# Optimization experiments

Measured on AMD Instinct MI355X. Metric: run time of the kernel, lower is better.

Reference implementation:

```python
import jax, jax.numpy as jnp
import numpy as np

BS, NS, NSTEP = 128, 1024, 8
IN_DIM, HID, MLP = 768, 512, 512
NEG = -100000.0


def setup_inputs() -> dict:
    key = jax.random.key(0)
    ks = jax.random.split(key, 12)
    s_h = 1.0 / np.sqrt(HID)
    s_cat = 1.0 / np.sqrt(HID + IN_DIM)
    s_m = 1.0 / np.sqrt(MLP)
    # gumbel noise implements Categorical sampling as argmax(logits + gumbel)
    u = jax.random.uniform(ks[9], (NSTEP, BS, NS), jnp.float32, 1e-7, 1.0 - 1e-7)
    return {
        "target_emb": jax.random.normal(ks[0], (BS, IN_DIM), jnp.float32),
        "ctx_emb": jax.random.normal(ks[1], (BS, NS, IN_DIM), jnp.float32),
        "target_len": jax.random.randint(ks[2], (BS,), 1, 32),
        "ctx_len": jax.random.randint(ks[3], (BS,), NSTEP, NS + 1),
        "n_step": NSTEP,
        "W_ih": jax.random.normal(ks[4], (4 * HID, IN_DIM), jnp.float32) * s_h,
        "W_hh": jax.random.normal(ks[5], (4 * HID, HID), jnp.float32) * s_h,
        "b_ih": jnp.zeros((4 * HID,), jnp.float32),
        "b_hh": jnp.zeros((4 * HID,), jnp.float32),
        "W1c": jax.random.normal(ks[6], (MLP, IN_DIM), jnp.float32) * s_cat,
        "W1h": jax.random.normal(ks[7], (MLP, HID), jnp.float32) * s_cat,
        "b1": jnp.zeros((MLP,), jnp.float32),
        "w2": jax.random.normal(ks[8], (MLP,), jnp.float32) * s_m,
        "b2": jnp.zeros((), jnp.float32),
        "gumbel": -jnp.log(-jnp.log(u)),
    }


def reference(target_emb, ctx_emb, target_len, ctx_len, n_step,
              W_ih, W_hh, b_ih, b_hh, W1c, W1h, b1, w2, b2, gumbel):
    bs, ns, in_dim = ctx_emb.shape
    hid = W_hh.shape[1]
    # mlp1 split: ctx part is constant across steps (concat([ctx, h]) @ W1^T = ctx@W1c^T + h@W1h^T)
    ctx_part = jnp.einsum('bnd,md->bnm', ctx_emb, W1c) + b1  # [bs, ns, mlp]
    mask0 = jnp.where(jnp.arange(ns)[None, :] >= ctx_len[:, None], NEG, 0.0).astype(jnp.float32)
    h0 = jnp.zeros((bs, hid), jnp.float32)
    c0 = jnp.zeros((bs, hid), jnp.float32)
    lp0 = jnp.zeros((bs,), jnp.float32)
    batch_idx = jnp.arange(bs)

    def step(carry, g):
        h, c, mask, x, lp = carry
        # LSTMCell (torch gate order: i, f, g, o); dropout is identity (eval semantics)
        gates = x @ W_ih.T + b_ih + h @ W_hh.T + b_hh
        i_g, f_g, g_g, o_g = jnp.split(gates, 4, axis=-1)
        c_new = jax.nn.sigmoid(f_g) * c + jax.nn.sigmoid(i_g) * jnp.tanh(g_g)
        h_new = jax.nn.sigmoid(o_g) * jnp.tanh(c_new)
        # attention-style MLP score
        pre = ctx_part + (h_new @ W1h.T)[:, None, :]          # [bs, ns, mlp]
        sc = jnp.tanh(pre) @ w2 + b2 + mask                   # [bs, ns]
        # Categorical(probs=softmax(sc)).sample() via Gumbel-argmax
        out = jnp.argmax(sc + g, axis=-1)                     # [bs]
        lp = lp + jnp.take_along_axis(jax.nn.log_softmax(sc, axis=-1), out[:, None], 1)[:, 0]
        mask = mask.at[batch_idx, out].set(NEG)
        x_new = jnp.take_along_axis(ctx_emb, out[:, None, None], axis=1)[:, 0, :]
        return (h_new, c_new, mask, x_new, lp), out

    (h, c, mask, x, log_probs), outputs = jax.lax.scan(
        step, (h0, c0, mask0, target_emb, lp0), gumbel)
    return outputs, log_probs
```

## Files before the change

### kernel.cpp

```cpp
#include <hip/hip_runtime.h>
#include <hip/hip_bf16.h>

#define BSZ 128
#define NSQ 1024
#define NSTEPC 8
#define IND 768
#define HIDD 512
#define G4D 2048
#define MLPD 512
#define KXD 1280
#define NEGV -100000.0f
#define KSG 16
#define KSH 8
#define MSPLIT 4

typedef __attribute__((ext_vector_type(4))) float f32x4;
typedef __attribute__((ext_vector_type(8))) short short8v;

__device__ __forceinline__ void gl16(const unsigned short* g, unsigned short* l) {
  __builtin_amdgcn_global_load_lds(
      (const __attribute__((address_space(1))) unsigned int*)(g),
      (__attribute__((address_space(3))) unsigned int*)(l), 16, 0, 0);
}

__device__ __forceinline__ void split2(float4 f0, float4 f1, short8v& hi, short8v& lo) {
  float fv[8] = {f0.x, f0.y, f0.z, f0.w, f1.x, f1.y, f1.z, f1.w};
#pragma unroll
  for (int j = 0; j < 8; ++j) {
    const unsigned ub = __builtin_bit_cast(unsigned, fv[j]);
    const unsigned hb = ub & 0xFFFF0000u;
    const float lf = fv[j] - __builtin_bit_cast(float, hb);
    hi[j] = (short)(hb >> 16);
    lo[j] = (short)(__builtin_bit_cast(unsigned, lf) >> 16);
  }
}

__device__ __forceinline__ float tanh_fast(float x) {
  x = fminf(fmaxf(x, -15.0f), 15.0f);
  float e = __builtin_amdgcn_exp2f(x * 2.8853900817779268f);
  float r = __builtin_amdgcn_rcpf(e + 1.0f);
  return fmaf(-2.0f, r, 1.0f);
}

__global__ __launch_bounds__(256) void k_prep_w1c(
    const float* __restrict__ W1c,
    unsigned short* __restrict__ wch, unsigned short* __restrict__ wcl) {
  const int c = blockIdx.x * 256 + threadIdx.x;
  if (c >= 49152) return;
  const int row = c / 96, wc = c - row * 96;
  const int tile = wc >> 2, c4 = wc & 3;
  const int slot = c4 ^ ((row >> 1) & 3);
  const size_t unit = ((size_t)((row >> 7) * 24 + tile) * 128 + (row & 127)) * 4 + slot;
  const float* src = W1c + (size_t)row * IND + wc * 8;
  const float4 f0 = *(const float4*)src, f1 = *(const float4*)(src + 4);
  short8v hi, lo;
  split2(f0, f1, hi, lo);
  *(short8v*)(wch + unit * 8) = hi;
  *(short8v*)(wcl + unit * 8) = lo;
}

__global__ __launch_bounds__(256) void k_init(
    const float* __restrict__ te, const int* __restrict__ cl,
    float* __restrict__ mask, float* __restrict__ xh,
    float* __restrict__ cst, float* __restrict__ lp) {
  const int b = blockIdx.x, tid = threadIdx.x;
  const int L = cl[b];
  for (int n = tid; n < NSQ; n += 256) mask[(size_t)b*NSQ + n] = (n >= L) ? NEGV : 0.0f;
  for (int d = tid; d < IND; d += 256) xh[(size_t)b*KXD + d] = te[(size_t)b*IND + d];
  for (int j = tid; j < HIDD; j += 256) {
    xh[(size_t)b*KXD + IND + j] = 0.0f;
    cst[(size_t)b*HIDD + j] = 0.0f;
  }
  if (tid == 0) lp[b] = 0.0f;
}

__global__ __launch_bounds__(256) void k_ctx5(
    const float* __restrict__ ctx,
    const unsigned short* __restrict__ wch, const unsigned short* __restrict__ wcl,
    const float* __restrict__ bias, const int* __restrict__ clen,
    float* __restrict__ cp) {
  __shared__ __align__(16) unsigned short sWh[2][4096], sWl[2][4096];
  __shared__ __align__(16) unsigned short sCh[2][4096], sCl[2][4096];
  const int bid = blockIdx.x;
  const int v = ((bid & 7) << 9) + (bid >> 3);
  const int mx = v & 3;
  const int rbC = v >> 2;
  const int b = rbC >> 3;
  const int nbase = (rbC & 7) << 7;
  if (nbase >= clen[b]) return;
  const int i0 = rbC << 7;
  const int m0 = mx << 7;
  const int tid = threadIdx.x;
  const int lane = tid & 63, wid = tid >> 6;
  const int wm = wid & 1, wn = wid >> 1;
  const int l15 = lane & 15, l4 = lane >> 4;
  const int c0r = tid >> 2, cs = tid & 3;
  const int c1r = 64 + c0r;
  const int k0rd = cs ^ ((c0r >> 1) & 3);
  const int k1rd = cs ^ ((c1r >> 1) & 3);
  const float* csrc0 = ctx + (size_t)(i0 + c0r) * IND + k0rd * 8;
  const float* csrc1 = ctx + (size_t)(i0 + c1r) * IND + k1rd * 8;

#pragma unroll
  for (int i = 0; i < 4; ++i) {
    const int seg = wid * 4 + i;
    const unsigned short* g = ((seg & 8) ? wcl : wch) +
        (size_t)(mx * 24) * 4096 + (seg & 7) * 512 + lane * 8;
    unsigned short* l = ((seg & 8) ? sWl[0] : sWh[0]) + (seg & 7) * 512;
    gl16(g, l);
  }
  {
    short8v hi, lo;
    split2(*(const float4*)csrc0, *(const float4*)(csrc0 + 4), hi, lo);
    *(short8v*)&sCh[0][tid * 8] = hi;
    *(short8v*)&sCl[0][tid * 8] = lo;
    split2(*(const float4*)csrc1, *(const float4*)(csrc1 + 4), hi, lo);
    *(short8v*)&sCh[0][(256 + tid) * 8] = hi;
    *(short8v*)&sCl[0][(256 + tid) * 8] = lo;
  }
  __syncthreads();

  f32x4 acc[4][4] = {};
  for (int t = 0; t < 24; ++t) {
    const int cur = t & 1, nb = cur ^ 1;
    float4 r00, r01, r10, r11;
    if (t + 1 < 24) {
#pragma unroll
      for (int i = 0; i < 4; ++i) {
        const int seg = wid * 4 + i;
        const unsigned short* g = ((seg & 8) ? wcl : wch) +
            (size_t)(mx * 24 + t + 1) * 4096 + (seg & 7) * 512 + lane * 8;
        unsigned short* l = ((seg & 8) ? sWl[nb] : sWh[nb]) + (seg & 7) * 512;
        gl16(g, l);
      }
      r00 = *(const float4*)(csrc0 + (t + 1) * 32);
      r01 = *(const float4*)(csrc0 + (t + 1) * 32 + 4);
      r10 = *(const float4*)(csrc1 + (t + 1) * 32);
      r11 = *(const float4*)(csrc1 + (t + 1) * 32 + 4);
    }
    short8v ah[4], al[4], bh[4], bl[4];
#pragma unroll
    for (int f = 0; f < 4; ++f) {
      const int rw = wm * 64 + f * 16 + l15;
      const int so = (l4 ^ ((rw >> 1) & 3)) << 3;
      ah[f] = *(const short8v*)&sWh[cur][rw * 32 + so];
      al[f] = *(const short8v*)&sWl[cur][rw * 32 + so];
      const int rc = wn * 64 + f * 16 + l15;
      const int sc = (l4 ^ ((rc >> 1) & 3)) << 3;
      bh[f] = *(const short8v*)&sCh[cur][rc * 32 + sc];
      bl[f] = *(const short8v*)&sCl[cur][rc * 32 + sc];
    }
#pragma unroll
    for (int fm = 0; fm < 4; ++fm)
#pragma unroll
      for (int fn = 0; fn < 4; ++fn) {
        acc[fm][fn] = __builtin_amdgcn_mfma_f32_16x16x32_bf16(ah[fm], bh[fn], acc[fm][fn], 0, 0, 0);
        acc[fm][fn] = __builtin_amdgcn_mfma_f32_16x16x32_bf16(ah[fm], bl[fn], acc[fm][fn], 0, 0, 0);
        acc[fm][fn] = __builtin_amdgcn_mfma_f32_16x16x32_bf16(al[fm], bh[fn], acc[fm][fn], 0, 0, 0);
      }
    if (t + 1 < 24) {
      short8v hi, lo;
      split2(r00, r01, hi, lo);
      *(short8v*)&sCh[nb][tid * 8] = hi;
      *(short8v*)&sCl[nb][tid * 8] = lo;
      split2(r10, r11, hi, lo);
      *(short8v*)&sCh[nb][(256 + tid) * 8] = hi;
      *(short8v*)&sCl[nb][(256 + tid) * 8] = lo;
    }
    __syncthreads();
  }
#pragma unroll
  for (int fm = 0; fm < 4; ++fm) {
#pragma unroll
    for (int r = 0; r < 4; ++r) {
      const int m = m0 + wm * 64 + fm * 16 + l4 * 4 + r;
      const float bb = bias[m];
      float* dst = cp + (((size_t)(b * MLPD + m)) << 10) + nbase + wn * 64 + l15;
#pragma unroll
      for (int fn = 0; fn < 4; ++fn)
        dst[fn * 16] = acc[fm][fn][r] + bb;
    }
  }
}

__global__ __launch_bounds__(256) void k_pgemm(
    const float* __restrict__ A, int lda, int acol,
    const float* __restrict__ B0, int ldb0, int kb,
    const float* __restrict__ B1, int ldb1,
    int kTiles, int N, float* __restrict__ P) {
  __shared__ float As[16][128];
  __shared__ float Bs[16][132];
  const int n0 = blockIdx.x * 128;
  const int kc0 = blockIdx.y * kTiles * 16;
  const int tid = threadIdx.x;
  const int tn = tid & 15;
  const int ta = tid >> 4;
  float acc[8][8] = {};
  for (int t = 0; t < kTiles; ++t) {
    const int k0 = kc0 + t * 16;
#pragma unroll
    for (int u = 0; u < 2; ++u) {
      const int v = tid + u * 256;
      const int r = v >> 2, kc = v & 3;
      const float4 a4 = *(const float4*)(A + (size_t)r * lda + acol + k0 + kc * 4);
      As[kc*4+0][r] = a4.x; As[kc*4+1][r] = a4.y; As[kc*4+2][r] = a4.z; As[kc*4+3][r] = a4.w;
      const float* bp = (k0 < kb) ? (B0 + (size_t)(n0 + r) * ldb0 + k0 + kc * 4)
                                  : (B1 + (size_t)(n0 + r) * ldb1 + (k0 - kb) + kc * 4);
      const float4 b4 = *(const float4*)bp;
      Bs[kc*4+0][r] = b4.x; Bs[kc*4+1][r] = b4.y; Bs[kc*4+2][r] = b4.z; Bs[kc*4+3][r] = b4.w;
    }
    __syncthreads();
#pragma unroll
    for (int kk = 0; kk < 16; ++kk) {
      float av[8], bv[8];
#pragma unroll
      for (int q = 0; q < 8; ++q) av[q] = As[kk][ta*8+q];
#pragma unroll
      for (int q = 0; q < 8; ++q) bv[q] = Bs[kk][tn*8+q];
#pragma unroll
      for (int ri = 0; ri < 8; ++ri)
#pragma unroll
        for (int ni = 0; ni < 8; ++ni)
          acc[ri][ni] = fmaf(av[ri], bv[ni], acc[ri][ni]);
    }
    __syncthreads();
  }
#pragma unroll
  for (int ri = 0; ri < 8; ++ri) {
    const int i = ta * 8 + ri;
    float* p = P + ((size_t)blockIdx.y * BSZ + i) * N + n0 + tn * 8;
    *(float4*)(p + 0) = make_float4(acc[ri][0], acc[ri][1], acc[ri][2], acc[ri][3]);
    *(float4*)(p + 4) = make_float4(acc[ri][4], acc[ri][5], acc[ri][6], acc[ri][7]);
  }
}

__global__ __launch_bounds__(512) void k_lstm(
    const float* __restrict__ gp, const float* __restrict__ b_ih,
    const float* __restrict__ b_hh, float* __restrict__ cst, float* __restrict__ xh) {
  const int b = blockIdx.x, j = threadIdx.x;
  float g[4];
#pragma unroll
  for (int q = 0; q < 4; ++q) {
    float s = b_ih[q*HIDD + j] + b_hh[q*HIDD + j];
#pragma unroll
    for (int ks = 0; ks < KSG; ++ks) s += gp[((size_t)ks*BSZ + b)*G4D + q*HIDD + j];
    g[q] = s;
  }
  const float c_old = cst[(size_t)b*HIDD + j];
  const float ig = 1.0f / (1.0f + expf(-g[0]));
  const float fg = 1.0f / (1.0f + expf(-g[1]));
  const float gg = tanhf(g[2]);
  const float og = 1.0f / (1.0f + expf(-g[3]));
  const float cn = fg * c_old + ig * gg;
  const float hn = og * tanhf(cn);
  cst[(size_t)b*HIDD + j] = cn;
  xh[(size_t)b*KXD + IND + j] = hn;
}

__global__ __launch_bounds__(256) void k_scores(
    const float* __restrict__ cp, const float* __restrict__ hpp,
    const float* __restrict__ w2, const int* __restrict__ clen,
    float* __restrict__ psc) {
  const int mh = blockIdx.x;
  const int b = blockIdx.y;
  const int tid = threadIdx.x;
  __shared__ float hs[128], ws[128];
  if (tid < 128) {
    const int m = mh * 128 + tid;
    float s = 0.0f;
#pragma unroll
    for (int ks = 0; ks < KSH; ++ks) s += hpp[((size_t)ks*BSZ + b)*MLPD + m];
    hs[tid] = s;
    ws[tid] = w2[m];
  }
  __syncthreads();
  const int len = clen[b];
  const int n0 = tid * 4;
  if (n0 >= len) return;
  float ax = 0, ay = 0, az = 0, aw = 0;
  const float* base = cp + ((size_t)b * MLPD + mh * 128) * NSQ + n0;
#pragma unroll 4
  for (int mm = 0; mm < 128; ++mm) {
    const float4 c4 = *(const float4*)(base + (size_t)mm * NSQ);
    const float h = hs[mm], w = ws[mm];
    ax = fmaf(tanh_fast(c4.x + h), w, ax);
    ay = fmaf(tanh_fast(c4.y + h), w, ay);
    az = fmaf(tanh_fast(c4.z + h), w, az);
    aw = fmaf(tanh_fast(c4.w + h), w, aw);
  }
  *(float4*)(psc + ((size_t)b * MSPLIT + mh) * NSQ + n0) = make_float4(ax, ay, az, aw);
}

__global__ __launch_bounds__(256) void k_argmax(
    const float* __restrict__ psc, float* __restrict__ mask,
    const float* __restrict__ gum, const float* __restrict__ b2p,
    float* __restrict__ lp, const float* __restrict__ ctx,
    float* __restrict__ xh, float* __restrict__ outv, int step) {
  const int b = blockIdx.x, tid = threadIdx.x;
  __shared__ float rv[256], rs[256], rm[256];
  __shared__ int ri[256];
  __shared__ int sel;
  const float b2 = b2p[0];
  const int n0 = tid * 4;
  const float4 m4 = *(const float4*)(mask + (size_t)b * NSQ + n0);
  float sc[4] = {b2 + m4.x, b2 + m4.y, b2 + m4.z, b2 + m4.w};
#pragma unroll
  for (int mh = 0; mh < MSPLIT; ++mh) {
    const float4 p4 = *(const float4*)(psc + ((size_t)b * MSPLIT + mh) * NSQ + n0);
    sc[0] += p4.x; sc[1] += p4.y; sc[2] += p4.z; sc[3] += p4.w;
  }
  const float4 g4 = *(const float4*)(gum + ((size_t)step * BSZ + b) * NSQ + n0);
  const float gv[4] = {g4.x, g4.y, g4.z, g4.w};
  float bestv = -1e30f, bests = 0.0f, msc = -1e30f;
  int bestn = 0;
#pragma unroll
  for (int q = 0; q < 4; ++q) {
    const float v = sc[q] + gv[q];
    if (v > bestv) { bestv = v; bestn = n0 + q; bests = sc[q]; }
    msc = fmaxf(msc, sc[q]);
  }
  rv[tid] = bestv; ri[tid] = bestn; rs[tid] = bests; rm[tid] = msc;
  __syncthreads();
  for (int o = 128; o > 0; o >>= 1) {
    if (tid < o) {
      if (rv[tid+o] > rv[tid] || (rv[tid+o] == rv[tid] && ri[tid+o] < ri[tid])) {
        rv[tid] = rv[tid+o]; ri[tid] = ri[tid+o]; rs[tid] = rs[tid+o];
      }
      rm[tid] = fmaxf(rm[tid], rm[tid+o]);
    }
    __syncthreads();
  }
  const float M = rm[0];
  __syncthreads();
  float se = 0.0f;
#pragma unroll
  for (int q = 0; q < 4; ++q)
    se += __builtin_amdgcn_exp2f((sc[q] - M) * 1.4426950408889634f);
  rm[tid] = se;
  __syncthreads();
  for (int o = 128; o > 0; o >>= 1) {
    if (tid < o) rm[tid] += rm[tid+o];
    __syncthreads();
  }
  if (tid == 0) {
    const int n = ri[0];
    const float lse = M + logf(rm[0]);
    const float nlp = lp[b] + rs[0] - lse;
    lp[b] = nlp;
    mask[(size_t)b * NSQ + n] = NEGV;
    outv[step * BSZ + b] = (float)n;
    if (step == NSTEPC - 1) outv[NSTEPC * BSZ + b] = nlp;
    sel = n;
  }
  __syncthreads();
  const int n = sel;
  const float4* src = (const float4*)(ctx + ((size_t)b * NSQ + n) * IND);
  float4* dst = (float4*)(xh + (size_t)b * KXD);
  for (int d = tid; d < IND / 4; d += 256) dst[d] = src[d];
}

extern "C" void kernel_launch(void* const* d_in, const int* in_sizes, int n_in,
                              void* d_out, int out_size, void* d_ws, size_t ws_size,
                              hipStream_t stream) {
  const float* target_emb = (const float*)d_in[0];
  const float* ctx_emb   = (const float*)d_in[1];
  const int*   ctx_len   = (const int*)d_in[3];
  const float* W_ih = (const float*)d_in[5];
  const float* W_hh = (const float*)d_in[6];
  const float* b_ih = (const float*)d_in[7];
  const float* b_hh = (const float*)d_in[8];
  const float* W1c  = (const float*)d_in[9];
  const float* W1h  = (const float*)d_in[10];
  const float* b1   = (const float*)d_in[11];
  const float* w2   = (const float*)d_in[12];
  const float* b2   = (const float*)d_in[13];
  const float* gumbel = (const float*)d_in[14];
  float* out = (float*)d_out;

  float* ws = (float*)d_ws;
  size_t off = 0;
  auto alloc = [&](size_t n) { float* p = ws + off; off += (n + 63) & ~(size_t)63; return p; };

  float* cp   = alloc((size_t)BSZ * MLPD * NSQ);
  float* gp   = alloc((size_t)KSG * BSZ * G4D);
  float* hpp  = alloc((size_t)KSH * BSZ * MLPD);
  float* psc  = alloc((size_t)BSZ * MSPLIT * NSQ);
  float* mask = alloc((size_t)BSZ * NSQ);
  float* xh   = alloc((size_t)BSZ * KXD);
  float* cst  = alloc((size_t)BSZ * HIDD);
  float* lp   = alloc(128);
  unsigned short* wch = (unsigned short*)alloc(196608);
  unsigned short* wcl = (unsigned short*)alloc(196608);

  k_prep_w1c<<<192, 256, 0, stream>>>(W1c, wch, wcl);
  k_init<<<BSZ, 256, 0, stream>>>(target_emb, ctx_len, mask, xh, cst, lp);
  k_ctx5<<<4096, 256, 0, stream>>>(ctx_emb, wch, wcl, b1, ctx_len, cp);

  for (int t = 0; t < NSTEPC; ++t) {
    k_pgemm<<<dim3(G4D/128, KSG), 256, 0, stream>>>(
        xh, KXD, 0, W_ih, IND, IND, W_hh, HIDD, 5, G4D, gp);
    k_lstm<<<BSZ, 512, 0, stream>>>(gp, b_ih, b_hh, cst, xh);
    k_pgemm<<<dim3(MLPD/128, KSH), 256, 0, stream>>>(
        xh, KXD, IND, W1h, HIDD, 1 << 30, nullptr, 0, 4, MLPD, hpp);
    k_scores<<<dim3(MSPLIT, BSZ), 256, 0, stream>>>(cp, hpp, w2, ctx_len, psc);
    k_argmax<<<BSZ, 256, 0, stream>>>(psc, mask, gumbel, b2, lp, ctx_emb, xh, out, t);
  }
}
```

Measured before the change: 857.7 us.

## Fuse LSTM cell, W1h projection, scoring and partial argmax into one kernel

Merges the LSTM cell, the h@W1h^T GEMM, the tanh-MLP scoring and the Gumbel argmax/log-sum-exp reduction into a single per-(batch, half) kernel. Each of 256 blocks recomputes the LSTM and the full W1h matvec in-block instead of running a split-K GEMM, then scores half of the context positions. A small pick kernel merges the two halves' partial max and sum-exp to finish the selection. This cuts three launches and several global round-trips per step. In exchange, the LSTM and W1h matvec work is done twice per batch row, and the W1h matvec uses a serial shuffle reduction per row.

```diff
diff --git a/kernel.cpp b/kernel.cpp
--- a/kernel.cpp
+++ b/kernel.cpp
@@ -11,8 +11,6 @@
 #define KXD 1280
 #define NEGV -100000.0f
 #define KSG 16
-#define KSH 8
-#define MSPLIT 4
 
 typedef __attribute__((ext_vector_type(4))) float f32x4;
 typedef __attribute__((ext_vector_type(8))) short short8v;
@@ -234,94 +232,119 @@
   }
 }
 
-__global__ __launch_bounds__(512) void k_lstm(
+__global__ __launch_bounds__(512) void k_mega(
     const float* __restrict__ gp, const float* __restrict__ b_ih,
-    const float* __restrict__ b_hh, float* __restrict__ cst, float* __restrict__ xh) {
-  const int b = blockIdx.x, j = threadIdx.x;
-  float g[4];
-#pragma unroll
-  for (int q = 0; q < 4; ++q) {
-    float s = b_ih[q*HIDD + j] + b_hh[q*HIDD + j];
-#pragma unroll
-    for (int ks = 0; ks < KSG; ++ks) s += gp[((size_t)ks*BSZ + b)*G4D + q*HIDD + j];
-    g[q] = s;
-  }
-  const float c_old = cst[(size_t)b*HIDD + j];
-  const float ig = 1.0f / (1.0f + expf(-g[0]));
-  const float fg = 1.0f / (1.0f + expf(-g[1]));
-  const float gg = tanhf(g[2]);
-  const float og = 1.0f / (1.0f + expf(-g[3]));
-  const float cn = fg * c_old + ig * gg;
-  const float hn = og * tanhf(cn);
-  cst[(size_t)b*HIDD + j] = cn;
-  xh[(size_t)b*KXD + IND + j] = hn;
-}
-
-__global__ __launch_bounds__(256) void k_scores(
-    const float* __restrict__ cp, const float* __restrict__ hpp,
-    const float* __restrict__ w2, const int* __restrict__ clen,
-    float* __restrict__ psc) {
-  const int mh = blockIdx.x;
-  const int b = blockIdx.y;
+    const float* __restrict__ b_hh, const float* __restrict__ W1h,
+    const float* __restrict__ w2, const float* __restrict__ b2p,
+    const int* __restrict__ clen, float* __restrict__ cst,
+    float* __restrict__ xh, const float* __restrict__ cp,
+    const float* __restrict__ mask, const float* __restrict__ gum,
+    float* __restrict__ part, int step) {
+  __shared__ float hs[HIDD];
+  __shared__ float hpw[MLPD];
+  __shared__ float w2s[MLPD];
+  __shared__ float4 ps4[4][128];
+  __shared__ float rv[128], rs[128], rm[128], r2[128];
+  __shared__ int ri[128];
+  const int b = blockIdx.x >> 1, half = blockIdx.x & 1;
   const int tid = threadIdx.x;
-  __shared__ float hs[128], ws[128];
+
+  {
+    float g[4];
+#pragma unroll
+    for (int q = 0; q < 4; ++q) {
+      float s = b_ih[q*HIDD + tid] + b_hh[q*HIDD + tid];
+#pragma unroll
+      for (int ks = 0; ks < KSG; ++ks)
+        s += gp[((size_t)ks*BSZ + b)*G4D + q*HIDD + tid];
+      g[q] = s;
+    }
+    const float c_old = cst[(size_t)b*HIDD + tid];
+    const float ig = 1.0f / (1.0f + expf(-g[0]));
+    const float fg = 1.0f / (1.0f + expf(-g[1]));
+    const float gg = tanhf(g[2]);
+    const float og = 1.0f / (1.0f + expf(-g[3]));
+    const float cn = fg * c_old + ig * gg;
+    const float hn = og * tanhf(cn);
+    if (half == 0) {
+      cst[(size_t)b*HIDD + tid] = cn;
+      xh[(size_t)b*KXD + IND + tid] = hn;
+    }
+    hs[tid] = hn;
+    w2s[tid] = w2[tid];
+  }
+  __syncthreads();
+
+  {
+    const int wv = tid >> 6, ln = tid & 63;
+    const float4 ha = *(const float4*)&hs[ln*8];
+    const float4 hb = *(const float4*)&hs[ln*8+4];
+    for (int i = 0; i < 64; ++i) {
+      const int row = wv * 64 + i;
+      const float* wr = W1h + (size_t)row * HIDD + ln * 8;
+      const float4 wa = *(const float4*)wr;
+      const float4 wb = *(const float4*)(wr + 4);
+      float p = wa.x*ha.x + wa.y*ha.y + wa.z*ha.z + wa.w*ha.w
+              + wb.x*hb.x + wb.y*hb.y + wb.z*hb.z + wb.w*hb.w;
+#pragma unroll
+      for (int o = 1; o < 64; o <<= 1) p += __shfl_xor(p, o);
+      if (ln == 0) hpw[row] = p;
+    }
+  }
+  __syncthreads();
+
+  const int len = clen[b];
+  {
+    const int mg = tid >> 7;
+    const int nc = tid & 127;
+    const int n0 = half * 512 + nc * 4;
+    float a0 = 0, a1 = 0, a2 = 0, a3 = 0;
+    if (n0 < len) {
+      const float* base = cp + ((size_t)(b * MLPD + mg * 128) << 10) + n0;
+      const float* hp = &hpw[mg * 128];
+      const float* wp = &w2s[mg * 128];
+#pragma unroll 8
+      for (int mm = 0; mm < 128; ++mm) {
+        const float4 c4 = *(const float4*)(base + ((size_t)mm << 10));
+        const float h = hp[mm], w = wp[mm];
+        a0 = fmaf(tanh_fast(c4.x + h), w, a0);
+        a1 = fmaf(tanh_fast(c4.y + h), w, a1);
+        a2 = fmaf(tanh_fast(c4.z + h), w, a2);
+        a3 = fmaf(tanh_fast(c4.w + h), w, a3);
+      }
+    }
+    ps4[mg][nc] = make_float4(a0, a1, a2, a3);
+  }
+  __syncthreads();
+
+  float sc[4];
   if (tid < 128) {
-    const int m = mh * 128 + tid;
-    float s = 0.0f;
-#pragma unroll
-    for (int ks = 0; ks < KSH; ++ks) s += hpp[((size_t)ks*BSZ + b)*MLPD + m];
-    hs[tid] = s;
-    ws[tid] = w2[m];
-  }
-  __syncthreads();
-  const int len = clen[b];
-  const int n0 = tid * 4;
-  if (n0 >= len) return;
-  float ax = 0, ay = 0, az = 0, aw = 0;
-  const float* base = cp + ((size_t)b * MLPD + mh * 128) * NSQ + n0;
-#pragma unroll 4
-  for (int mm = 0; mm < 128; ++mm) {
-    const float4 c4 = *(const float4*)(base + (size_t)mm * NSQ);
-    const float h = hs[mm], w = ws[mm];
-    ax = fmaf(tanh_fast(c4.x + h), w, ax);
-    ay = fmaf(tanh_fast(c4.y + h), w, ay);
-    az = fmaf(tanh_fast(c4.z + h), w, az);
-    aw = fmaf(tanh_fast(c4.w + h), w, aw);
-  }
-  *(float4*)(psc + ((size_t)b * MSPLIT + mh) * NSQ + n0) = make_float4(ax, ay, az, aw);
-}
-
-__global__ __launch_bounds__(256) void k_argmax(
-    const float* __restrict__ psc, float* __restrict__ mask,
-    const float* __restrict__ gum, const float* __restrict__ b2p,
-    float* __restrict__ lp, const float* __restrict__ ctx,
-    float* __restrict__ xh, float* __restrict__ outv, int step) {
-  const int b = blockIdx.x, tid = threadIdx.x;
-  __shared__ float rv[256], rs[256], rm[256];
-  __shared__ int ri[256];
-  __shared__ int sel;
-  const float b2 = b2p[0];
-  const int n0 = tid * 4;
-  const float4 m4 = *(const float4*)(mask + (size_t)b * NSQ + n0);
-  float sc[4] = {b2 + m4.x, b2 + m4.y, b2 + m4.z, b2 + m4.w};
-#pragma unroll
-  for (int mh = 0; mh < MSPLIT; ++mh) {
-    const float4 p4 = *(const float4*)(psc + ((size_t)b * MSPLIT + mh) * NSQ + n0);
-    sc[0] += p4.x; sc[1] += p4.y; sc[2] += p4.z; sc[3] += p4.w;
-  }
-  const float4 g4 = *(const float4*)(gum + ((size_t)step * BSZ + b) * NSQ + n0);
-  const float gv[4] = {g4.x, g4.y, g4.z, g4.w};
-  float bestv = -1e30f, bests = 0.0f, msc = -1e30f;
-  int bestn = 0;
-#pragma unroll
-  for (int q = 0; q < 4; ++q) {
-    const float v = sc[q] + gv[q];
-    if (v > bestv) { bestv = v; bestn = n0 + q; bests = sc[q]; }
-    msc = fmaxf(msc, sc[q]);
-  }
-  rv[tid] = bestv; ri[tid] = bestn; rs[tid] = bests; rm[tid] = msc;
-  __syncthreads();
-  for (int o = 128; o > 0; o >>= 1) {
+    const int n0 = half * 512 + tid * 4;
+    if (n0 < len) {
+      const float4 p0 = ps4[0][tid], p1 = ps4[1][tid], p2 = ps4[2][tid], p3 = ps4[3][tid];
+      const float b2 = b2p[0];
+      const float4 m4 = *(const float4*)(mask + (size_t)b * NSQ + n0);
+      sc[0] = p0.x + p1.x + p2.x + p3.x + b2 + m4.x;
+      sc[1] = p0.y + p1.y + p2.y + p3.y + b2 + m4.y;
+      sc[2] = p0.z + p1.z + p2.z + p3.z + b2 + m4.z;
+      sc[3] = p0.w + p1.w + p2.w + p3.w + b2 + m4.w;
+    } else {
+      sc[0] = sc[1] = sc[2] = sc[3] = -1e30f;
+    }
+    const float4 g4 = *(const float4*)(gum + ((size_t)step * BSZ + b) * NSQ + n0);
+    const float gv[4] = {g4.x, g4.y, g4.z, g4.w};
+    float bestv = -1e30f, bests = 0.0f, msc = -1e30f;
+    int bestn = 0;
+#pragma unroll
+    for (int q = 0; q < 4; ++q) {
+      const float vv = sc[q] + gv[q];
+      if (vv > bestv) { bestv = vv; bestn = n0 + q; bests = sc[q]; }
+      msc = fmaxf(msc, sc[q]);
+    }
+    rv[tid] = bestv; ri[tid] = bestn; rs[tid] = bests; rm[tid] = msc;
+  }
+  __syncthreads();
+  for (int o = 64; o > 0; o >>= 1) {
     if (tid < o) {
       if (rv[tid+o] > rv[tid] || (rv[tid+o] == rv[tid] && ri[tid+o] < ri[tid])) {
         rv[tid] = rv[tid+o]; ri[tid] = ri[tid+o]; rs[tid] = rs[tid+o];
@@ -331,21 +354,40 @@
     __syncthreads();
   }
   const float M = rm[0];
-  __syncthreads();
-  float se = 0.0f;
-#pragma unroll
-  for (int q = 0; q < 4; ++q)
-    se += __builtin_amdgcn_exp2f((sc[q] - M) * 1.4426950408889634f);
-  rm[tid] = se;
-  __syncthreads();
-  for (int o = 128; o > 0; o >>= 1) {
-    if (tid < o) rm[tid] += rm[tid+o];
+  if (tid < 128) {
+    float se = 0.0f;
+#pragma unroll
+    for (int q = 0; q < 4; ++q)
+      se += __builtin_amdgcn_exp2f((sc[q] - M) * 1.4426950408889634f);
+    r2[tid] = se;
+  }
+  __syncthreads();
+  for (int o = 64; o > 0; o >>= 1) {
+    if (tid < o) r2[tid] += r2[tid+o];
     __syncthreads();
   }
   if (tid == 0) {
-    const int n = ri[0];
-    const float lse = M + logf(rm[0]);
-    const float nlp = lp[b] + rs[0] - lse;
+    float* p = part + (size_t)(b * 2 + half) * 8;
+    p[0] = rv[0]; p[1] = (float)ri[0]; p[2] = rs[0]; p[3] = M; p[4] = r2[0];
+  }
+}
+
+__global__ __launch_bounds__(192) void k_pick(
+    const float* __restrict__ part, float* __restrict__ mask,
+    float* __restrict__ lp, const float* __restrict__ ctx,
+    float* __restrict__ xh, float* __restrict__ outv, int step) {
+  const int b = blockIdx.x, tid = threadIdx.x;
+  __shared__ int sel;
+  if (tid == 0) {
+    const float* p0 = part + (size_t)(b * 2) * 8;
+    const float* p1 = p0 + 8;
+    int n; float bests;
+    if (p1[0] > p0[0]) { n = (int)p1[1]; bests = p1[2]; }
+    else               { n = (int)p0[1]; bests = p0[2]; }
+    const float M0 = p0[3], M1 = p1[3];
+    const float M = fmaxf(M0, M1);
+    const float S = p0[4] * expf(M0 - M) + p1[4] * expf(M1 - M);
+    const float nlp = lp[b] + bests - (M + logf(S));
     lp[b] = nlp;
     mask[(size_t)b * NSQ + n] = NEGV;
     outv[step * BSZ + b] = (float)n;
@@ -356,7 +398,7 @@
   const int n = sel;
   const float4* src = (const float4*)(ctx + ((size_t)b * NSQ + n) * IND);
   float4* dst = (float4*)(xh + (size_t)b * KXD);
-  for (int d = tid; d < IND / 4; d += 256) dst[d] = src[d];
+  dst[tid] = src[tid];
 }
 
 extern "C" void kernel_launch(void* const* d_in, const int* in_sizes, int n_in,
@@ -383,12 +425,11 @@
 
   float* cp   = alloc((size_t)BSZ * MLPD * NSQ);
   float* gp   = alloc((size_t)KSG * BSZ * G4D);
-  float* hpp  = alloc((size_t)KSH * BSZ * MLPD);
-  float* psc  = alloc((size_t)BSZ * MSPLIT * NSQ);
   float* mask = alloc((size_t)BSZ * NSQ);
   float* xh   = alloc((size_t)BSZ * KXD);
   float* cst  = alloc((size_t)BSZ * HIDD);
   float* lp   = alloc(128);
+  float* part = alloc(BSZ * 2 * 8);
   unsigned short* wch = (unsigned short*)alloc(196608);
   unsigned short* wcl = (unsigned short*)alloc(196608);
 
@@ -399,10 +440,9 @@
   for (int t = 0; t < NSTEPC; ++t) {
     k_pgemm<<<dim3(G4D/128, KSG), 256, 0, stream>>>(
         xh, KXD, 0, W_ih, IND, IND, W_hh, HIDD, 5, G4D, gp);
-    k_lstm<<<BSZ, 512, 0, stream>>>(gp, b_ih, b_hh, cst, xh);
-    k_pgemm<<<dim3(MLPD/128, KSH), 256, 0, stream>>>(
-        xh, KXD, IND, W1h, HIDD, 1 << 30, nullptr, 0, 4, MLPD, hpp);
-    k_scores<<<dim3(MSPLIT, BSZ), 256, 0, stream>>>(cp, hpp, w2, ctx_len, psc);
-    k_argmax<<<BSZ, 256, 0, stream>>>(psc, mask, gumbel, b2, lp, ctx_emb, xh, out, t);
-  }
-}
+    k_mega<<<BSZ * 2, 512, 0, stream>>>(
+        gp, b_ih, b_hh, W1h, w2, b2, ctx_len, cst, xh, cp, mask,
+        gumbel, part, t);
+    k_pick<<<BSZ, 192, 0, stream>>>(part, mask, lp, ctx_emb, xh, out, t);
+  }
+}
```

Result: slower. 1.005 ms (+17.1%).
